# Kernel optimization log

Measured on AMD Instinct MI355X. Metric: run time of the kernel, lower is better.

Reference implementation:

```python
import jax, jax.numpy as jnp
import numpy as np


def setup_inputs() -> dict:
    key = jax.random.key(0)
    ks = jax.random.split(key, 7)
    B, H, W = 32, 28, 28
    C3, C4 = 1024, 2048
    C = C3 + C4            # 3072
    L1 = 9                 # num_landmarks + 1
    A, NC = 312, 200
    return {
        "l3": jax.random.normal(ks[0], (B, C3, H, W), jnp.float32),
        "l4": jax.random.normal(ks[1], (B, C4, H // 2, W // 2), jnp.float32),
        "conv_w": jax.random.normal(ks[2], (L1, C), jnp.float32) * 0.02,
        "modulation": jnp.ones((1, C, L1), jnp.float32),
        "attr_w": jax.random.normal(ks[3], (A, C), jnp.float32) * 0.02,
        "attr_b": jnp.zeros((A,), jnp.float32),
        "class_w": jax.random.normal(ks[4], (NC, A), jnp.float32) * 0.02,
    }


def reference(l3, l4, conv_w, modulation, attr_w, attr_b, class_w):
    b, c3, h, w = l3.shape
    # F.interpolate(l4, (h, w), mode='bilinear', align_corners=False)
    l4_up = jax.image.resize(l4, (b, l4.shape[1], h, w), method="bilinear")
    x = jnp.concatenate([l4_up, l3], axis=1)            # (b, 3072, h, w)

    # 1x1 conv: ab[b,l,h,w] = sum_c w[l,c] * x[b,c,h,w]
    ab = jnp.einsum("lc,bchw->blhw", conv_w, x)
    b_sq = jnp.sum(x * x, axis=1, keepdims=True)        # (b,1,h,w)
    a_sq = jnp.sum(conv_w, axis=1)[None, :, None, None]  # (1,L+1,1,1)  (matches torch: weight.sum(1), NOT squared)
    maps = jax.nn.softmax(-(b_sq - 2.0 * ab + a_sq), axis=1)  # Softmax2d = softmax over channels

    # (maps[:,None] * x[:,:,None]).mean((-1,-2))  ->  batched GEMM over spatial dim
    all_features = jnp.einsum("blhw,bchw->bcl", maps, x) / (h * w)  # (b, c, L+1)

    mod = all_features * modulation                     # dropout is identity at eval
    # permute(0,2,1)[:, :-1, :].mean(1) == mean over landmark dim excluding background
    mean_features = jnp.mean(mod[:, :, :-1], axis=2)    # (b, c)

    attr_scores = mean_features @ attr_w.T + attr_b      # (b, 312)
    class_scores = attr_scores @ class_w.T               # (b, 200)
    return attr_scores, class_scores, maps, all_features
```

## Files before the change

kernel.cpp:

```cpp
#include <hip/hip_runtime.h>
#include <math.h>

#define B_    32
#define C3_   1024
#define C4_   2048
#define C_    3072
#define P_    784
#define Q_    196
#define L_    9
#define NG_   25088
#define A_    312
#define NC_   200

#define ATTR_OFF  0
#define CLASS_OFF 9984
#define MAPS_OFF  16384
#define AF_OFF    242176

#define ASQ_OFF   0
#define MF_OFF    16
#define LOGITS_OFF 98320
#define Y_OFF     (LOGITS_OFF + 9 * NG_)
#define MP_OFF    (Y_OFF + 32 * 9 * Q_)

typedef __attribute__((ext_vector_type(8))) short bf16x8;
typedef __attribute__((ext_vector_type(4))) float f32x4;

__device__ __forceinline__ short f2bf(float f) {
    union { float f; unsigned u; } v; v.f = f;
    unsigned r = v.u + 0x7FFFu + ((v.u >> 16) & 1u);
    return (short)(r >> 16);
}

#define GLDS16(gp, lp) __builtin_amdgcn_global_load_lds(                    \
        (const __attribute__((address_space(1))) unsigned int*)(gp),        \
        (__attribute__((address_space(3))) unsigned int*)(lp), 16, 0, 0)

__global__ __launch_bounds__(256) void zK(const float* __restrict__ conv_w,
                                          float* __restrict__ Y,
                                          float* __restrict__ logits,
                                          float* __restrict__ asq) {
    if (blockIdx.x == 0) {
        __shared__ float red[256];
        int t = threadIdx.x;
        for (int l = 0; l < L_; ++l) {
            float s = 0.f;
            for (int c = t; c < C_; c += 256) s += conv_w[l * C_ + c];
            red[t] = s; __syncthreads();
            for (int o = 128; o > 0; o >>= 1) {
                if (t < o) red[t] += red[t + o];
                __syncthreads();
            }
            if (t == 0) asq[l] = red[0];
            __syncthreads();
        }
        return;
    }
    int i = (blockIdx.x - 1) * 256 + threadIdx.x;
    if (i < 32 * 9 * Q_) Y[i] = 0.f;
    else if (i < 32 * 9 * Q_ + 9 * NG_) logits[i - 32 * 9 * Q_] = 0.f;
}

__global__ __launch_bounds__(256, 5) void kA(
        const float* __restrict__ l3, const float* __restrict__ l4,
        const float* __restrict__ conv_w,
        float* __restrict__ logits, float* __restrict__ Y) {
    __shared__ float X[2][16 * 256];
    int bid = blockIdx.x;
    int t = threadIdx.x;
    int wave = t >> 6, lane = t & 63;

    bool isl3 = (bid < 1568);
    int slab = 0, g0 = 0, b = 0, grp = 0, cbase_w;
    const float* gbase;
    size_t rowpitch;
    if (isl3) {
        slab = bid / 98;
        g0 = (bid % 98) * 256;
        int gidx = g0 + lane * 4;
        int bb = gidx / 784, px = gidx % 784;
        gbase = l3 + ((size_t)bb * C3_ + slab * 64) * P_ + px;
        rowpitch = P_;
        cbase_w = C4_ + slab * 64;
    } else {
        int idx = bid - 1568;
        b = idx >> 5; grp = idx & 31;
        int q = lane * 4;
        if (q > 192) q = 192;
        gbase = l4 + ((size_t)b * C4_ + grp * 64) * Q_ + q;
        rowpitch = Q_;
        cbase_w = grp * 64;
    }

#pragma unroll
    for (int r = 0; r < 4; ++r) {
        int row = wave * 4 + r;
        GLDS16(gbase + (size_t)row * rowpitch, &X[0][row * 256]);
    }

    float acc[9];
#pragma unroll
    for (int l = 0; l < 9; ++l) acc[l] = 0.f;

#pragma unroll
    for (int j = 0; j < 4; ++j) {
        const int cur = j & 1;
        if (j < 3) {
#pragma unroll
            for (int r = 0; r < 4; ++r) {
                int row = wave * 4 + r;
                int ch = (j + 1) * 16 + row;
                GLDS16(gbase + (size_t)ch * rowpitch, &X[cur ^ 1][row * 256]);
            }
            asm volatile("s_waitcnt vmcnt(4)" ::: "memory");
        } else {
            asm volatile("s_waitcnt vmcnt(0)" ::: "memory");
        }
        __builtin_amdgcn_s_barrier();

        if (isl3 || t < 196) {
#pragma unroll
            for (int c = 0; c < 16; ++c) {
                float x = X[cur][c * 256 + t];
#pragma unroll
                for (int l = 0; l < 9; ++l)
                    acc[l] = fmaf(conv_w[(size_t)l * C_ + cbase_w + j * 16 + c],
                                  x, acc[l]);
            }
        }
        __builtin_amdgcn_s_barrier();
    }

    if (isl3) {
#pragma unroll
        for (int l = 0; l < 9; ++l)
            atomicAdd(&logits[(size_t)l * NG_ + g0 + t], 2.f * acc[l]);
    } else if (t < 196) {
#pragma unroll
        for (int l = 0; l < 9; ++l)
            atomicAdd(&Y[((size_t)b * 9 + l) * Q_ + t], acc[l]);
    }
}

__global__ __launch_bounds__(256) void kC(const float* __restrict__ logits,
                                          const float* __restrict__ Y,
                                          const float* __restrict__ asq,
                                          float* __restrict__ out_maps) {
    int g = blockIdx.x * 256 + threadIdx.x;
    int b = g / P_, p = g % P_;
    int yy = p / 28, xx = p % 28;
    float sy = 0.5f * yy - 0.25f, sx = 0.5f * xx - 0.25f;
    float fyf = floorf(sy), fxf = floorf(sx);
    float fy = sy - fyf, fx = sx - fxf;
    int ya = max(0, (int)fyf), yb = min(13, (int)fyf + 1);
    int xa = max(0, (int)fxf), xb = min(13, (int)fxf + 1);
    float w00 = (1.f - fy) * (1.f - fx), w01 = (1.f - fy) * fx;
    float w10 = fy * (1.f - fx),         w11 = fy * fx;
    float v[9];
#pragma unroll
    for (int l = 0; l < 9; ++l) {
        const float* Yl = Y + ((size_t)b * 9 + l) * Q_;
        float ab4 = w00 * Yl[ya * 14 + xa] + w01 * Yl[ya * 14 + xb]
                  + w10 * Yl[yb * 14 + xa] + w11 * Yl[yb * 14 + xb];
        v[l] = logits[(size_t)l * NG_ + g] + 2.f * ab4 - asq[l];
    }
    float m = v[0];
#pragma unroll
    for (int l = 1; l < 9; ++l) m = fmaxf(m, v[l]);
    float sum = 0.f;
#pragma unroll
    for (int l = 0; l < 9; ++l) { v[l] = expf(v[l] - m); sum += v[l]; }
    float inv = 1.f / sum;
#pragma unroll
    for (int l = 0; l < 9; ++l)
        out_maps[(size_t)b * (L_ * P_) + l * P_ + p] = v[l] * inv;
}

__device__ __forceinline__ int adj_taps(int q, int* ys, float* wy) {
    if (q == 0)  { ys[0] = 0;  wy[0] = 1.00f; ys[1] = 1;  wy[1] = 0.75f;
                   ys[2] = 2;  wy[2] = 0.25f; return 3; }
    if (q == 13) { ys[0] = 25; wy[0] = 0.25f; ys[1] = 26; wy[1] = 0.75f;
                   ys[2] = 27; wy[2] = 1.00f; return 3; }
    ys[0] = 2 * q - 1; wy[0] = 0.25f;
    ys[1] = 2 * q;     wy[1] = 0.75f;
    ys[2] = 2 * q + 1; wy[2] = 0.75f;
    ys[3] = 2 * q + 2; wy[3] = 0.25f;
    return 4;
}

__global__ __launch_bounds__(256) void kD(const float* __restrict__ maps,
                                          float* __restrict__ Mp) {
    int tid = blockIdx.x * 256 + threadIdx.x;
    if (tid >= 32 * 9 * Q_) return;
    int b = tid / (9 * Q_);
    int r = tid % (9 * Q_);
    int l = r / Q_, q = r % Q_;
    int qy = q / 14, qx = q % 14;
    int ys[4], xs[4]; float wy[4], wx[4];
    int ny = adj_taps(qy, ys, wy);
    int nx = adj_taps(qx, xs, wx);
    const float* mrow = maps + (size_t)b * (L_ * P_) + l * P_;
    float s = 0.f;
    for (int i = 0; i < ny; ++i) {
        float rs = 0.f;
        for (int j = 0; j < nx; ++j)
            rs = fmaf(wx[j], mrow[ys[i] * 28 + xs[j]], rs);
        s = fmaf(wy[i], rs, s);
    }
    Mp[(size_t)b * (9 * Q_) + r] = s;
}

#define SA 232
__global__ __launch_bounds__(256, 2) void kE(
        const float* __restrict__ l3, const float* __restrict__ l4,
        const float* __restrict__ maps, const float* __restrict__ Mp,
        const float* __restrict__ mod,
        float* __restrict__ out_af, float* __restrict__ mf) {
    __shared__ short As[2][64 * SA];
    __shared__ short Bs[2][16 * SA];
    int bid = blockIdx.x;
    int t = threadIdx.x;
    int wave = t >> 6, lane = t & 63;
    int row16 = lane & 15, quad = lane >> 4;

    bool isl3 = (bid < 512);
    int b, c0, nchunk, cglob0, pitch;
    const float* xsrc; const float* bsrc;
    if (isl3) {
        b = bid >> 4; c0 = (bid & 15) * 64; nchunk = 4;
        xsrc = l3 + ((size_t)b * C3_ + c0) * P_;
        bsrc = maps + (size_t)b * (L_ * P_);
        pitch = P_;
        cglob0 = C4_ + c0;
    } else {
        int idx = bid - 512;
        b = idx >> 5; c0 = (idx & 31) * 64; nchunk = 1;
        xsrc = l4 + ((size_t)b * C4_ + c0) * Q_;
        bsrc = Mp + (size_t)b * (9 * Q_);
        pitch = Q_;
        cglob0 = c0;
    }

#pragma unroll
    for (int it = 0; it < 5; ++it) {
        int i = t + it * 256;
        if (i < 1152) {
            int br = i / 9;
            int j = 196 + (i % 9) * 4;
            *(ushort4*)(&As[br >> 6][(br & 63) * SA + j]) =
                make_ushort4(0, 0, 0, 0);
        }
    }

    auto stage = [&](int cc, int buf) {
        int koff = cc * 196;
        float4 va[13];
#pragma unroll
        for (int it = 0; it < 13; ++it) {
            int i = t + it * 256;
            if (i < 3136) {
                int r = i / 49, j = (i % 49) * 4;
                va[it] = *(const float4*)(xsrc + (size_t)r * pitch + koff + j);
            }
        }
        float4 vb[4];
#pragma unroll
        for (int it = 0; it < 4; ++it) {
            int i = t + it * 256;
            if (i < 928) {
                int r = i / 58, j = (i % 58) * 4;
                if (r < 9 && j < 196)
                    vb[it] = *(const float4*)(bsrc + (size_t)r * pitch + koff + j);
                else
                    vb[it] = make_float4(0.f, 0.f, 0.f, 0.f);
            }
        }
#pragma unroll
        for (int it = 0; it < 13; ++it) {
            int i = t + it * 256;
            if (i < 3136) {
                int r = i / 49, j = (i % 49) * 4;
                ushort4 o;
                o.x = (unsigned short)f2bf(va[it].x);
                o.y = (unsigned short)f2bf(va[it].y);
                o.z = (unsigned short)f2bf(va[it].z);
                o.w = (unsigned short)f2bf(va[it].w);
                *(ushort4*)(&As[buf][r * SA + j]) = o;
            }
        }
#pragma unroll
        for (int it = 0; it < 4; ++it) {
            int i = t + it * 256;
            if (i < 928) {
                int r = i / 58, j = (i % 58) * 4;
                ushort4 o;
                o.x = (unsigned short)f2bf(vb[it].x);
                o.y = (unsigned short)f2bf(vb[it].y);
                o.z = (unsigned short)f2bf(vb[it].z);
                o.w = (unsigned short)f2bf(vb[it].w);
                *(ushort4*)(&Bs[buf][r * SA + j]) = o;
            }
        }
    };

    stage(0, 0);
    __syncthreads();

    f32x4 acc = {0.f, 0.f, 0.f, 0.f};
    for (int cc = 0; cc < nchunk; ++cc) {
        int cur = cc & 1;
        if (cc + 1 < nchunk) stage(cc + 1, cur ^ 1);
        const short* arow = &As[cur][(wave * 16 + row16) * SA];
        const short* brow = &Bs[cur][row16 * SA];
#pragma unroll
        for (int k0 = 0; k0 < 224; k0 += 32) {
            bf16x8 a = *(const bf16x8*)(arow + k0 + quad * 8);
            bf16x8 bv = *(const bf16x8*)(brow + k0 + quad * 8);
            acc = __builtin_amdgcn_mfma_f32_16x16x32_bf16(a, bv, acc, 0, 0, 0);
        }
        __syncthreads();
    }

    int l = row16;
    int cg = cglob0 + wave * 16 + quad * 4;
    float afv[4];
#pragma unroll
    for (int r = 0; r < 4; ++r) afv[r] = acc[r] * (1.f / 784.f);
    if (l < 9) {
        size_t base = ((size_t)b * C_ + cg) * 9 + l;
#pragma unroll
        for (int r = 0; r < 4; ++r) out_af[base + (size_t)r * 9] = afv[r];
    }
    float term[4];
#pragma unroll
    for (int r = 0; r < 4; ++r)
        term[r] = (l < 8) ? afv[r] * mod[(size_t)(cg + r) * 9 + l] : 0.f;
#pragma unroll
    for (int s = 1; s < 16; s <<= 1)
#pragma unroll
        for (int r = 0; r < 4; ++r) term[r] += __shfl_xor(term[r], s);
    if (row16 == 0) {
#pragma unroll
        for (int r = 0; r < 4; ++r)
            mf[(size_t)b * C_ + cg + r] = term[r] * 0.125f;
    }
}

__global__ __launch_bounds__(256) void kF(
        const float* __restrict__ mf, const float* __restrict__ attr_w,
        const float* __restrict__ attr_b, float* __restrict__ out_attr) {
    int idx = blockIdx.x * 4 + (threadIdx.x >> 6);
    int lane = threadIdx.x & 63;
    int b = idx / A_, a = idx % A_;
    const float4* wr = (const float4*)(attr_w + (size_t)a * C_);
    const float4* mr = (const float4*)(mf + (size_t)b * C_);
    float acc = 0.f;
    for (int j = lane; j < C_ / 4; j += 64) {
        float4 w = wr[j], m = mr[j];
        acc += w.x * m.x + w.y * m.y + w.z * m.z + w.w * m.w;
    }
    acc += __shfl_xor(acc, 1);  acc += __shfl_xor(acc, 2);
    acc += __shfl_xor(acc, 4);  acc += __shfl_xor(acc, 8);
    acc += __shfl_xor(acc, 16); acc += __shfl_xor(acc, 32);
    if (lane == 0) out_attr[idx] = acc + attr_b[a];
}

__global__ __launch_bounds__(256) void kG(
        const float* __restrict__ attr, const float* __restrict__ class_w,
        float* __restrict__ out_class) {
    int idx = blockIdx.x * 4 + (threadIdx.x >> 6);
    int lane = threadIdx.x & 63;
    int b = idx / NC_, n = idx % NC_;
    float acc = 0.f;
    for (int a = lane; a < A_; a += 64)
        acc += attr[b * A_ + a] * class_w[n * A_ + a];
    acc += __shfl_xor(acc, 1);  acc += __shfl_xor(acc, 2);
    acc += __shfl_xor(acc, 4);  acc += __shfl_xor(acc, 8);
    acc += __shfl_xor(acc, 16); acc += __shfl_xor(acc, 32);
    if (lane == 0) out_class[idx] = acc;
}

extern "C" void kernel_launch(void* const* d_in, const int* in_sizes, int n_in,
                              void* d_out, int out_size, void* d_ws, size_t ws_size,
                              hipStream_t stream) {
    (void)in_sizes; (void)n_in; (void)out_size; (void)ws_size;
    const float* l3         = (const float*)d_in[0];
    const float* l4         = (const float*)d_in[1];
    const float* conv_w     = (const float*)d_in[2];
    const float* modulation = (const float*)d_in[3];
    const float* attr_w     = (const float*)d_in[4];
    const float* attr_b     = (const float*)d_in[5];
    const float* class_w    = (const float*)d_in[6];
    float* out = (float*)d_out;
    float* ws  = (float*)d_ws;
    float* asq    = ws + ASQ_OFF;
    float* mf     = ws + MF_OFF;
    float* logits = ws + LOGITS_OFF;
    float* Y      = ws + Y_OFF;
    float* Mp     = ws + MP_OFF;

    zK<<<1104, 256, 0, stream>>>(conv_w, Y, logits, asq);
    kA<<<2592, 256, 0, stream>>>(l3, l4, conv_w, logits, Y);
    kC<<<98, 256, 0, stream>>>(logits, Y, asq, out + MAPS_OFF);
    kD<<<221, 256, 0, stream>>>(out + MAPS_OFF, Mp);
    kE<<<1536, 256, 0, stream>>>(l3, l4, out + MAPS_OFF, Mp, modulation,
                                 out + AF_OFF, mf);
    kF<<<(B_ * A_) / 4, 256, 0, stream>>>(mf, attr_w, attr_b, out + ATTR_OFF);
    kG<<<(B_ * NC_) / 4, 256, 0, stream>>>(out + ATTR_OFF, class_w,
                                           out + CLASS_OFF);
}
```

Baseline: 312.5 us.

## Stage kE inputs via per-wave direct global-to-LDS loads, drop block syncs

Replaces the block-wide double-buffered bf16 staging of kE with per-wave fp32 tiles loaded directly into LDS through a GLDS16 global-to-LDS path. Each wave then converts to bf16 at MFMA operand load time, and the B operand is read from global straight into registers. This removes __syncthreads and the register round-trip for conversion. Occupancy rises to 3 blocks per SM and the l4 blocks are scheduled first. In exchange, the per-chunk loads are no longer overlapped with compute, and the fp32 LDS footprint is larger.

```diff
diff --git a/kernel.cpp b/kernel.cpp
--- a/kernel.cpp
+++ b/kernel.cpp
@@ -210,115 +210,96 @@
     Mp[(size_t)b * (9 * Q_) + r] = s;
 }
 
-#define SA 232
-__global__ __launch_bounds__(256, 2) void kE(
+#define WREG 3328
+__global__ __launch_bounds__(256, 3) void kE(
         const float* __restrict__ l3, const float* __restrict__ l4,
         const float* __restrict__ maps, const float* __restrict__ Mp,
         const float* __restrict__ mod,
         float* __restrict__ out_af, float* __restrict__ mf) {
-    __shared__ short As[2][64 * SA];
-    __shared__ short Bs[2][16 * SA];
+    __shared__ float X[4 * WREG];
     int bid = blockIdx.x;
     int t = threadIdx.x;
     int wave = t >> 6, lane = t & 63;
     int row16 = lane & 15, quad = lane >> 4;
 
-    bool isl3 = (bid < 512);
+    bool isl4 = (bid < 1024);
     int b, c0, nchunk, cglob0, pitch;
     const float* xsrc; const float* bsrc;
-    if (isl3) {
-        b = bid >> 4; c0 = (bid & 15) * 64; nchunk = 4;
+    if (isl4) {
+        b = bid >> 5; c0 = (bid & 31) * 64; nchunk = 1;
+        xsrc = l4 + ((size_t)b * C4_ + c0) * Q_;
+        bsrc = Mp + (size_t)b * (9 * Q_);
+        pitch = Q_;
+        cglob0 = c0;
+    } else {
+        int idx = bid - 1024;
+        b = idx >> 4; c0 = (idx & 15) * 64; nchunk = 4;
         xsrc = l3 + ((size_t)b * C3_ + c0) * P_;
         bsrc = maps + (size_t)b * (L_ * P_);
         pitch = P_;
         cglob0 = C4_ + c0;
-    } else {
-        int idx = bid - 512;
-        b = idx >> 5; c0 = (idx & 31) * 64; nchunk = 1;
-        xsrc = l4 + ((size_t)b * C4_ + c0) * Q_;
-        bsrc = Mp + (size_t)b * (9 * Q_);
-        pitch = Q_;
-        cglob0 = c0;
-    }
-
-#pragma unroll
-    for (int it = 0; it < 5; ++it) {
-        int i = t + it * 256;
-        if (i < 1152) {
-            int br = i / 9;
-            int j = 196 + (i % 9) * 4;
-            *(ushort4*)(&As[br >> 6][(br & 63) * SA + j]) =
-                make_ushort4(0, 0, 0, 0);
-        }
-    }
-
-    auto stage = [&](int cc, int buf) {
-        int koff = cc * 196;
-        float4 va[13];
-#pragma unroll
-        for (int it = 0; it < 13; ++it) {
-            int i = t + it * 256;
-            if (i < 3136) {
-                int r = i / 49, j = (i % 49) * 4;
-                va[it] = *(const float4*)(xsrc + (size_t)r * pitch + koff + j);
-            }
-        }
-        float4 vb[4];
-#pragma unroll
-        for (int it = 0; it < 4; ++it) {
-            int i = t + it * 256;
-            if (i < 928) {
-                int r = i / 58, j = (i % 58) * 4;
-                if (r < 9 && j < 196)
-                    vb[it] = *(const float4*)(bsrc + (size_t)r * pitch + koff + j);
-                else
-                    vb[it] = make_float4(0.f, 0.f, 0.f, 0.f);
-            }
-        }
-#pragma unroll
-        for (int it = 0; it < 13; ++it) {
-            int i = t + it * 256;
-            if (i < 3136) {
-                int r = i / 49, j = (i % 49) * 4;
-                ushort4 o;
-                o.x = (unsigned short)f2bf(va[it].x);
-                o.y = (unsigned short)f2bf(va[it].y);
-                o.z = (unsigned short)f2bf(va[it].z);
-                o.w = (unsigned short)f2bf(va[it].w);
-                *(ushort4*)(&As[buf][r * SA + j]) = o;
-            }
-        }
-#pragma unroll
-        for (int it = 0; it < 4; ++it) {
-            int i = t + it * 256;
-            if (i < 928) {
-                int r = i / 58, j = (i % 58) * 4;
-                ushort4 o;
-                o.x = (unsigned short)f2bf(vb[it].x);
-                o.y = (unsigned short)f2bf(vb[it].y);
-                o.z = (unsigned short)f2bf(vb[it].z);
-                o.w = (unsigned short)f2bf(vb[it].w);
-                *(ushort4*)(&Bs[buf][r * SA + j]) = o;
-            }
-        }
-    };
-
-    stage(0, 0);
-    __syncthreads();
+    }
+    const float* wrow = xsrc + (size_t)(wave * 16) * pitch;
+    float* Xw = X + wave * WREG;
 
     f32x4 acc = {0.f, 0.f, 0.f, 0.f};
-    for (int cc = 0; cc < nchunk; ++cc) {
-        int cur = cc & 1;
-        if (cc + 1 < nchunk) stage(cc + 1, cur ^ 1);
-        const short* arow = &As[cur][(wave * 16 + row16) * SA];
-        const short* brow = &Bs[cur][row16 * SA];
-#pragma unroll
-        for (int k0 = 0; k0 < 224; k0 += 32) {
-            bf16x8 a = *(const bf16x8*)(arow + k0 + quad * 8);
-            bf16x8 bv = *(const bf16x8*)(brow + k0 + quad * 8);
-            acc = __builtin_amdgcn_mfma_f32_16x16x32_bf16(a, bv, acc, 0, 0, 0);
-        }
-        __syncthreads();
+    for (int h = 0; h < nchunk; ++h) {
+        int koff = h * 196;
+#pragma unroll
+        for (int k = 0; k < 13; ++k) {
+            int f = k * 256 + lane * 4;
+            if (f > 3132) f = 3132;
+            int r = f / 196, j = f % 196;
+            GLDS16(wrow + (size_t)r * pitch + koff + j, &Xw[k * 256]);
+        }
+        bf16x8 bfr[7];
+#pragma unroll
+        for (int s = 0; s < 7; ++s) {
+            int k0 = s * 32 + quad * 8;
+            bf16x8 bv = {0, 0, 0, 0, 0, 0, 0, 0};
+            if (row16 < 9) {
+                const float* bp = bsrc + (size_t)row16 * pitch + koff + k0;
+                if (s < 6) {
+                    float4 b0 = *(const float4*)(bp);
+                    float4 b1 = *(const float4*)(bp + 4);
+                    bv[0] = f2bf(b0.x); bv[1] = f2bf(b0.y);
+                    bv[2] = f2bf(b0.z); bv[3] = f2bf(b0.w);
+                    bv[4] = f2bf(b1.x); bv[5] = f2bf(b1.y);
+                    bv[6] = f2bf(b1.z); bv[7] = f2bf(b1.w);
+                } else if (quad == 0) {
+                    float4 b0 = *(const float4*)(bp);
+                    bv[0] = f2bf(b0.x); bv[1] = f2bf(b0.y);
+                    bv[2] = f2bf(b0.z); bv[3] = f2bf(b0.w);
+                }
+            }
+            bfr[s] = bv;
+        }
+        asm volatile("s_waitcnt vmcnt(0)" ::: "memory");
+
+#pragma unroll
+        for (int s = 0; s < 7; ++s) {
+            int k0 = s * 32 + quad * 8;
+            bf16x8 av = {0, 0, 0, 0, 0, 0, 0, 0};
+            const float* ap = Xw + row16 * 196 + k0;
+            if (s < 6) {
+                float4 a0 = *(const float4*)(ap);
+                float4 a1 = *(const float4*)(ap + 4);
+                av[0] = f2bf(a0.x); av[1] = f2bf(a0.y);
+                av[2] = f2bf(a0.z); av[3] = f2bf(a0.w);
+                av[4] = f2bf(a1.x); av[5] = f2bf(a1.y);
+                av[6] = f2bf(a1.z); av[7] = f2bf(a1.w);
+            } else if (quad == 0) {
+                float4 a0 = *(const float4*)(ap);
+                av[0] = f2bf(a0.x); av[1] = f2bf(a0.y);
+                av[2] = f2bf(a0.z); av[3] = f2bf(a0.w);
+            }
+            acc = __builtin_amdgcn_mfma_f32_16x16x32_bf16(av, bfr[s], acc,
+                                                          0, 0, 0);
+        }
+        if (h + 1 < nchunk) {
+            asm volatile("s_waitcnt lgkmcnt(0)" ::: "memory");
+            __builtin_amdgcn_sched_barrier(0);
+        }
     }
 
     int l = row16;
```

Result: slower. 323.4 us (+3.5%).
